# Optimization experiments

Hardware: AMD Instinct MI355X
Metric: run time of the kernel (lower is better)

Reference implementation:

```python
import jax, jax.numpy as jnp
import numpy as np

N_NODES = 200000
N_EDGES = 6400000
NUM_GRAPHS = 20000
D_NODE, D_EDGE, D_MSG = 5, 4, 10


def setup_inputs() -> dict:
    key = jax.random.key(0)
    ks = jax.random.split(key, 16)
    inp = {
        "edge_index": jax.random.randint(ks[0], (2, N_EDGES), 0, N_NODES, dtype=jnp.int64)
                      if jax.config.jax_enable_x64 else
                      jax.random.randint(ks[0], (2, N_EDGES), 0, N_NODES, dtype=jnp.int32),
        "node_attr": jax.random.normal(ks[1], (N_NODES, D_NODE), dtype=jnp.float32),
        "edge_attr": jax.random.normal(ks[2], (N_EDGES, D_EDGE), dtype=jnp.float32),
        "batch": jnp.sort(jax.random.randint(ks[3], (N_NODES,), 0, NUM_GRAPHS, dtype=jnp.int32)),
        "num_graphs": NUM_GRAPHS,
        # MPL_1: Linear(2*D_NODE + D_EDGE -> 10)
        "w_mpl": jax.random.normal(ks[4], (2 * D_NODE + D_EDGE, D_MSG), dtype=jnp.float32) * 0.3,
        "b_mpl": jnp.zeros((D_MSG,), dtype=jnp.float32),
        "w1": jax.random.normal(ks[5], (10, 10), dtype=jnp.float32) * 0.3,
        "b1": jnp.zeros((10,), dtype=jnp.float32),
        "w2": jax.random.normal(ks[6], (10, 5), dtype=jnp.float32) * 0.3,
        "b2": jnp.zeros((5,), dtype=jnp.float32),
        "w3": jax.random.normal(ks[7], (5, 5), dtype=jnp.float32) * 0.3,
        "b3": jnp.zeros((5,), dtype=jnp.float32),
        "w4": jax.random.normal(ks[8], (5, 1), dtype=jnp.float32) * 0.3,
        "b4": jnp.zeros((1,), dtype=jnp.float32),
    }
    return inp


def reference(edge_index, node_attr, edge_attr, batch, num_graphs,
              w_mpl, b_mpl, w1, b1, w2, b2, w3, b3, w4, b4):
    src, dst = edge_index[0], edge_index[1]
    n_nodes = node_attr.shape[0]
    # MPL_1: gather endpoints, concat with edge features, MLP, scatter-sum to dst
    edge_in = jnp.concatenate(
        [node_attr[src], node_attr[dst], edge_attr], axis=-1)  # [E, 14]
    msg = jax.nn.relu(edge_in @ w_mpl + b_mpl)                 # [E, 10]
    x = jax.ops.segment_sum(msg, dst, num_segments=n_nodes)    # [N, 10]
    # node MLP head
    x = jax.nn.relu(x @ w1 + b1)
    x = jax.nn.relu(x @ w2 + b2)
    # segment_coo(reduce='sum') over sorted batch index -> per-graph pooling
    x = jax.ops.segment_sum(x, batch, num_segments=num_graphs,
                            indices_are_sorted=True)           # [G, 5]
    x = jax.nn.relu(x @ w3 + b3)
    return x @ w4 + b4                                         # [G, 1]
```

## Files before the change

kernel.cpp:

```cpp
#include <hip/hip_runtime.h>

#define DN 5
#define DE 4
#define DM 10
#define NB 2048
#define BKT_SH 8
#define BKT_NODES 256
#define MAXBKT 1024

__global__ __launch_bounds__(256) void hist_pack_kernel(
    const int* __restrict__ ei, const float* __restrict__ node_attr,
    float4* __restrict__ napack, unsigned* __restrict__ cnt,
    int E, int chunk, int nbk, int N)
{
    __shared__ unsigned hist[MAXBKT];
    int t = threadIdx.x, b = blockIdx.x;

    int n = b * 256 + t;
    if (n < N) {
        const float* r = node_attr + (size_t)n * DN;
        napack[2 * (size_t)n]     = make_float4(r[0], r[1], r[2], r[3]);
        napack[2 * (size_t)n + 1] = make_float4(r[4], 0.f, 0.f, 0.f);
    }

    for (int j = t; j < nbk; j += 256) hist[j] = 0;
    __syncthreads();

    int e0 = b * chunk, e1 = min(E, e0 + chunk);
    for (int i = e0 + t; i < e1; i += 256) {
        int d = ei[(size_t)E + i];
        atomicAdd(&hist[d >> BKT_SH], 1u);
    }
    __syncthreads();
    for (int j = t; j < nbk; j += 256)
        cnt[(size_t)j * NB + b] = hist[j];
}

__global__ __launch_bounds__(256) void scan_rows_kernel(
    unsigned* __restrict__ cnt, unsigned* __restrict__ rowtotal)
{
    __shared__ unsigned lds[256];
    int j = blockIdx.x, t = threadIdx.x;
    unsigned* row = cnt + (size_t)j * NB;

    unsigned v[8], s = 0;
#pragma unroll
    for (int u = 0; u < 8; ++u) { v[u] = row[t * 8 + u]; s += v[u]; }
    lds[t] = s; __syncthreads();
#pragma unroll
    for (int o = 1; o < 256; o <<= 1) {
        unsigned add = (t >= o) ? lds[t - o] : 0u;
        __syncthreads();
        lds[t] += add;
        __syncthreads();
    }
    unsigned excl = lds[t] - s;
#pragma unroll
    for (int u = 0; u < 8; ++u) { row[t * 8 + u] = excl; excl += v[u]; }
    if (t == 255) rowtotal[j] = lds[255];
}

__global__ __launch_bounds__(1024) void scan_base_kernel(
    const unsigned* __restrict__ rowtotal, unsigned* __restrict__ gbase,
    int nbk, int E)
{
    __shared__ unsigned lds[1024];
    int t = threadIdx.x;
    unsigned v = (t < nbk) ? rowtotal[t] : 0u;
    lds[t] = v; __syncthreads();
#pragma unroll
    for (int o = 1; o < 1024; o <<= 1) {
        unsigned add = (t >= o) ? lds[t - o] : 0u;
        __syncthreads();
        lds[t] += add;
        __syncthreads();
    }
    unsigned excl = lds[t] - v;
    if (t < nbk)       gbase[t] = excl;
    else if (t == nbk) gbase[t] = (unsigned)E;
}

__global__ __launch_bounds__(256) void scatter_kernel(
    const int* __restrict__ ei, const float* __restrict__ edge_attr,
    const unsigned* __restrict__ cnt, const unsigned* __restrict__ gbase,
    float4* __restrict__ rec4, int E, int chunk, int nbk)
{
    __shared__ unsigned woff[MAXBKT];
    int t = threadIdx.x, b = blockIdx.x;
    for (int j = t; j < nbk; j += 256)
        woff[j] = gbase[j] + cnt[(size_t)j * NB + b];
    __syncthreads();

    int e0 = b * chunk, e1 = min(E, e0 + chunk);
    for (int i0 = e0 + t; i0 < e1; i0 += 4 * 256) {
        int s[4], d[4]; float4 ea[4]; bool act[4];
#pragma unroll
        for (int u = 0; u < 4; ++u) {
            int i = i0 + u * 256;
            act[u] = (i < e1);
            if (act[u]) {
                s[u] = ei[i];
                d[u] = ei[(size_t)E + i];
                ea[u] = reinterpret_cast<const float4*>(edge_attr)[i];
            }
        }
#pragma unroll
        for (int u = 0; u < 4; ++u) {
            if (!act[u]) continue;
            unsigned p = atomicAdd(&woff[d[u] >> BKT_SH], 1u);
            unsigned meta = (unsigned)s[u] | ((unsigned)(d[u] & 255) << 18);
            rec4[2 * (size_t)p]     = make_float4(__uint_as_float(meta), ea[u].x, ea[u].y, ea[u].z);
            rec4[2 * (size_t)p + 1] = make_float4(ea[u].w, 0.f, 0.f, 0.f);
        }
    }
}

__global__ __launch_bounds__(256) void gather_kernel(
    const float4* __restrict__ rec4, const unsigned* __restrict__ gbase,
    const float4* __restrict__ napack,
    const float* __restrict__ w_mpl, const float* __restrict__ b_mpl,
    float* __restrict__ xpart, size_t xstride,
    int E, int N, int nbk, int nsplit)
{
    __shared__ float acc[BKT_NODES * DM];
    __shared__ float pdl[BKT_NODES * 12];
    __shared__ float sws[50];
    __shared__ float swe[40];

    int t = threadIdx.x;
    int j  = blockIdx.x / nsplit;
    int sp = blockIdx.x - j * nsplit;
    int nb0 = j * BKT_NODES;

    if (t < 50)       sws[t] = w_mpl[t];
    else if (t < 90)  swe[t - 50] = w_mpl[100 + (t - 50)];

    for (int i = t; i < BKT_NODES * DM; i += 256) acc[i] = 0.f;

    {
        int n = nb0 + t;
        float a0 = 0.f, a1 = 0.f, a2 = 0.f, a3 = 0.f, a4 = 0.f;
        if (n < N) {
            float4 r0 = napack[2 * (size_t)n];
            float4 r1 = napack[2 * (size_t)n + 1];
            a0 = r0.x; a1 = r0.y; a2 = r0.z; a3 = r0.w; a4 = r1.x;
        }
#pragma unroll
        for (int q = 0; q < DM; ++q) {
            float v = b_mpl[q];
            v = fmaf(a0, w_mpl[50 + q], v);
            v = fmaf(a1, w_mpl[60 + q], v);
            v = fmaf(a2, w_mpl[70 + q], v);
            v = fmaf(a3, w_mpl[80 + q], v);
            v = fmaf(a4, w_mpl[90 + q], v);
            pdl[t * 12 + q] = v;
        }
    }
    __syncthreads();

    unsigned start = gbase[j];
    unsigned end   = gbase[j + 1];
    unsigned blen  = end - start;
    unsigned csz   = (blen + nsplit - 1) / nsplit;
    unsigned ss    = start + (unsigned)sp * csz;
    unsigned se    = min(end, ss + csz);

    for (unsigned i0 = ss + t; i0 < se; i0 += 4u * 256u) {
        float4 r0[4], r1[4]; bool act[4];
#pragma unroll
        for (int u = 0; u < 4; ++u) {
            unsigned i = i0 + (unsigned)u * 256u;
            act[u] = (i < se);
            if (act[u]) { r0[u] = rec4[2 * (size_t)i]; r1[u] = rec4[2 * (size_t)i + 1]; }
        }
        float4 n0[4], n1[4];
#pragma unroll
        for (int u = 0; u < 4; ++u)
            if (act[u]) {
                size_t s = __float_as_uint(r0[u].x) & 0x3FFFFu;
                n0[u] = napack[2 * s];
                n1[u] = napack[2 * s + 1];
            }
#pragma unroll
        for (int u = 0; u < 4; ++u) {
            if (!act[u]) continue;
            unsigned meta = __float_as_uint(r0[u].x);
            int dl = meta >> 18;
            const float* pr = &pdl[dl * 12];
            float4 p0 = *reinterpret_cast<const float4*>(pr);
            float4 p1 = *reinterpret_cast<const float4*>(pr + 4);
            float2 p2 = *reinterpret_cast<const float2*>(pr + 8);
            float m[DM] = {p0.x, p0.y, p0.z, p0.w, p1.x, p1.y, p1.z, p1.w, p2.x, p2.y};
            float a0 = n0[u].x, a1 = n0[u].y, a2 = n0[u].z, a3 = n0[u].w, a4 = n1[u].x;
            float e0 = r0[u].y, e1 = r0[u].z, e2 = r0[u].w, e3 = r1[u].x;
#pragma unroll
            for (int q = 0; q < DM; ++q) {
                float v = m[q];
                v = fmaf(a0, sws[q],      v);
                v = fmaf(a1, sws[10 + q], v);
                v = fmaf(a2, sws[20 + q], v);
                v = fmaf(a3, sws[30 + q], v);
                v = fmaf(a4, sws[40 + q], v);
                v = fmaf(e0, swe[q],      v);
                v = fmaf(e1, swe[10 + q], v);
                v = fmaf(e2, swe[20 + q], v);
                v = fmaf(e3, swe[30 + q], v);
                if (v > 0.f) atomicAdd(&acc[dl * DM + q], v);
            }
        }
    }
    __syncthreads();

    float* dst = xpart + (size_t)sp * xstride + (size_t)nb0 * DM;
    for (int i = t; i < BKT_NODES * DM; i += 256) dst[i] = acc[i];
}

__global__ __launch_bounds__(256) void combine_kernel(
    const float* __restrict__ xpart, size_t xstride,
    const int* __restrict__ batch,
    const float* __restrict__ w1, const float* __restrict__ b1,
    const float* __restrict__ w2, const float* __restrict__ b2,
    float* __restrict__ gacc, int N, int nsplit)
{
    __shared__ float s1[100], sb1[10], s2[50], sb2[5];
    int t = threadIdx.x;
    if (t < 100)      s1[t] = w1[t];
    else if (t < 110) sb1[t - 100] = b1[t - 100];
    else if (t < 160) s2[t - 110] = w2[t - 110];
    else if (t < 165) sb2[t - 160] = b2[t - 160];
    __syncthreads();

    int n = blockIdx.x * blockDim.x + t;
    bool valid = (n < N);
    int g = 0x7fffffff;
    float h2[5] = {0.f, 0.f, 0.f, 0.f, 0.f};

    if (valid) {
        float x[DM];
#pragma unroll
        for (int q = 0; q < DM; ++q) x[q] = 0.f;
        for (int sp = 0; sp < nsplit; ++sp) {
            const float2* row = reinterpret_cast<const float2*>(
                xpart + (size_t)sp * xstride + (size_t)n * DM);
#pragma unroll
            for (int h = 0; h < 5; ++h) {
                float2 v = row[h];
                x[2 * h] += v.x; x[2 * h + 1] += v.y;
            }
        }

        float h1[10];
#pragma unroll
        for (int q = 0; q < 10; ++q) h1[q] = sb1[q];
#pragma unroll
        for (int k = 0; k < 10; ++k)
#pragma unroll
            for (int q = 0; q < 10; ++q) h1[q] = fmaf(x[k], s1[k * 10 + q], h1[q]);
#pragma unroll
        for (int q = 0; q < 10; ++q) h1[q] = fmaxf(h1[q], 0.f);
#pragma unroll
        for (int q = 0; q < 5; ++q) h2[q] = sb2[q];
#pragma unroll
        for (int k = 0; k < 10; ++k)
#pragma unroll
            for (int q = 0; q < 5; ++q) h2[q] = fmaf(h1[k], s2[k * 5 + q], h2[q]);
#pragma unroll
        for (int q = 0; q < 5; ++q) h2[q] = fmaxf(h2[q], 0.f);
        g = batch[n];
    }

    int lane = t & 63;
#pragma unroll
    for (int o = 1; o < 64; o <<= 1) {
        int go = __shfl_down(g, o);
        float v0 = __shfl_down(h2[0], o);
        float v1 = __shfl_down(h2[1], o);
        float v2 = __shfl_down(h2[2], o);
        float v3 = __shfl_down(h2[3], o);
        float v4 = __shfl_down(h2[4], o);
        if (lane + o < 64 && go == g) {
            h2[0] += v0; h2[1] += v1; h2[2] += v2; h2[3] += v3; h2[4] += v4;
        }
    }
    int gp = __shfl_up(g, 1);
    bool head = (lane == 0) || (gp != g);
    if (head && g != 0x7fffffff) {
#pragma unroll
        for (int q = 0; q < 5; ++q)
            if (h2[q] != 0.f) unsafeAtomicAdd(&gacc[(size_t)g * 5 + q], h2[q]);
    }
}

__global__ __launch_bounds__(256) void graph_head_kernel(
    const float* __restrict__ gacc,
    const float* __restrict__ w3, const float* __restrict__ b3,
    const float* __restrict__ w4, const float* __restrict__ b4,
    float* __restrict__ out, int G)
{
    __shared__ float s3[25], sb3[5], s4[5], sb4[1];
    int t = threadIdx.x;
    if (t < 25)       s3[t] = w3[t];
    else if (t < 30)  sb3[t - 25] = b3[t - 25];
    else if (t < 35)  s4[t - 30] = w4[t - 30];
    else if (t == 35) sb4[0] = b4[0];
    __syncthreads();

    int g = blockIdx.x * blockDim.x + t;
    if (g >= G) return;

    float x[5];
#pragma unroll
    for (int k = 0; k < 5; ++k) x[k] = gacc[(size_t)g * 5 + k];

    float o = sb4[0];
#pragma unroll
    for (int q = 0; q < 5; ++q) {
        float h = sb3[q];
#pragma unroll
        for (int k = 0; k < 5; ++k) h = fmaf(x[k], s3[k * 5 + q], h);
        h = fmaxf(h, 0.f);
        o = fmaf(h, s4[q], o);
    }
    out[g] = o;
}

extern "C" void kernel_launch(void* const* d_in, const int* in_sizes, int n_in,
                              void* d_out, int out_size, void* d_ws, size_t ws_size,
                              hipStream_t stream)
{
    const int*   ei        = (const int*)d_in[0];
    const float* node_attr = (const float*)d_in[1];
    const float* edge_attr = (const float*)d_in[2];
    const int*   batch     = (const int*)d_in[3];
    const float* w_mpl = (const float*)d_in[5];
    const float* b_mpl = (const float*)d_in[6];
    const float* w1    = (const float*)d_in[7];
    const float* b1    = (const float*)d_in[8];
    const float* w2    = (const float*)d_in[9];
    const float* b2    = (const float*)d_in[10];
    const float* w3    = (const float*)d_in[11];
    const float* b3    = (const float*)d_in[12];
    const float* w4    = (const float*)d_in[13];
    const float* b4    = (const float*)d_in[14];
    float* out = (float*)d_out;

    const int E = in_sizes[0] / 2;
    const int N = in_sizes[1] / DN;
    const int G = out_size;

    const int nbk   = (N + BKT_NODES - 1) / BKT_NODES;
    const int chunk = (E + NB - 1) / NB;

    char* p = (char*)d_ws;
    float4*   rec4     = (float4*)p;   p += (size_t)E * 32;
    float4*   napack   = (float4*)p;   p += (size_t)N * 32;
    unsigned* rowtotal = (unsigned*)p; p += ((size_t)nbk * 4 + 15) & ~15ull;
    unsigned* gbase    = (unsigned*)p; p += ((size_t)(nbk + 1) * 4 + 15) & ~15ull;
    float*    gacc     = (float*)p;    p += (size_t)G * 5 * 4;
    unsigned* cnt      = (unsigned*)p;
    float*    xpart    = (float*)p;
    size_t cnt_bytes = (size_t)nbk * NB * 4;

    size_t used = (size_t)((char*)cnt - (char*)d_ws);
    size_t xstride = (size_t)nbk * BKT_NODES * DM;
    int nsplit = 8;
    while (nsplit > 1 &&
           used + ((cnt_bytes > (size_t)nsplit * xstride * 4) ? cnt_bytes
                                                              : (size_t)nsplit * xstride * 4) > ws_size)
        nsplit >>= 1;

    hipMemsetAsync(gacc, 0, (size_t)G * 5 * 4, stream);

    hist_pack_kernel<<<NB, 256, 0, stream>>>(ei, node_attr, napack, cnt, E, chunk, nbk, N);
    scan_rows_kernel<<<nbk, 256, 0, stream>>>(cnt, rowtotal);
    scan_base_kernel<<<1, 1024, 0, stream>>>(rowtotal, gbase, nbk, E);
    scatter_kernel<<<NB, 256, 0, stream>>>(ei, edge_attr, cnt, gbase, rec4, E, chunk, nbk);
    gather_kernel<<<nbk * nsplit, 256, 0, stream>>>(rec4, gbase, napack, w_mpl, b_mpl,
                                                    xpart, xstride, E, N, nbk, nsplit);
    combine_kernel<<<nbk, 256, 0, stream>>>(xpart, xstride, batch, w1, b1, w2, b2, gacc, N, nsplit);
    graph_head_kernel<<<(G + 255) / 256, 256, 0, stream>>>(gacc, w3, b3, w4, b4, out, G);
}
```

Measured before the change: 585.1 us.

## Prefetch source node features into edge records as fp16 during scatter

The scatter pass now gathers each edge's source-node features and stores them in the bucketed edge record alongside the edge attributes. Both are converted to half precision, so the gather pass no longer does random node lookups. Node packs shrink to 16 bytes, and nontemporal loads and stores are used for streaming data. This trades fp16 rounding of the inputs for fewer random reads and less data per record.

```diff
diff --git a/kernel.cpp b/kernel.cpp
--- a/kernel.cpp
+++ b/kernel.cpp
@@ -1,4 +1,5 @@
 #include <hip/hip_runtime.h>
+#include <hip/hip_fp16.h>
 
 #define DN 5
 #define DE 4
@@ -8,9 +9,21 @@
 #define BKT_NODES 256
 #define MAXBKT 1024
 
+typedef float        f4  __attribute__((ext_vector_type(4)));
+typedef unsigned int u4v __attribute__((ext_vector_type(4)));
+
+static __device__ __forceinline__ float2 h2f(unsigned u) {
+    __half2 h = *reinterpret_cast<__half2*>(&u);
+    return make_float2(__low2float(h), __high2float(h));
+}
+static __device__ __forceinline__ unsigned f2h(float a, float b) {
+    __half2 h = __floats2half2_rn(a, b);
+    return *reinterpret_cast<unsigned*>(&h);
+}
+
 __global__ __launch_bounds__(256) void hist_pack_kernel(
     const int* __restrict__ ei, const float* __restrict__ node_attr,
-    float4* __restrict__ napack, unsigned* __restrict__ cnt,
+    u4v* __restrict__ naph, unsigned* __restrict__ cnt,
     int E, int chunk, int nbk, int N)
 {
     __shared__ unsigned hist[MAXBKT];
@@ -19,8 +32,12 @@
     int n = b * 256 + t;
     if (n < N) {
         const float* r = node_attr + (size_t)n * DN;
-        napack[2 * (size_t)n]     = make_float4(r[0], r[1], r[2], r[3]);
-        napack[2 * (size_t)n + 1] = make_float4(r[4], 0.f, 0.f, 0.f);
+        u4v v;
+        v.x = f2h(r[0], r[1]);
+        v.y = f2h(r[2], r[3]);
+        v.z = f2h(r[4], 0.f);
+        v.w = 0u;
+        naph[n] = v;
     }
 
     for (int j = t; j < nbk; j += 256) hist[j] = 0;
@@ -28,7 +45,7 @@
 
     int e0 = b * chunk, e1 = min(E, e0 + chunk);
     for (int i = e0 + t; i < e1; i += 256) {
-        int d = ei[(size_t)E + i];
+        int d = __builtin_nontemporal_load(ei + (size_t)E + i);
         atomicAdd(&hist[d >> BKT_SH], 1u);
     }
     __syncthreads();
@@ -83,7 +100,8 @@
 __global__ __launch_bounds__(256) void scatter_kernel(
     const int* __restrict__ ei, const float* __restrict__ edge_attr,
     const unsigned* __restrict__ cnt, const unsigned* __restrict__ gbase,
-    float4* __restrict__ rec4, int E, int chunk, int nbk)
+    const u4v* __restrict__ naph,
+    f4* __restrict__ rec, int E, int chunk, int nbk)
 {
     __shared__ unsigned woff[MAXBKT];
     int t = threadIdx.x, b = blockIdx.x;
@@ -93,31 +111,43 @@
 
     int e0 = b * chunk, e1 = min(E, e0 + chunk);
     for (int i0 = e0 + t; i0 < e1; i0 += 4 * 256) {
-        int s[4], d[4]; float4 ea[4]; bool act[4];
+        int s[4], d[4]; f4 ea[4]; bool act[4];
 #pragma unroll
         for (int u = 0; u < 4; ++u) {
             int i = i0 + u * 256;
             act[u] = (i < e1);
             if (act[u]) {
-                s[u] = ei[i];
-                d[u] = ei[(size_t)E + i];
-                ea[u] = reinterpret_cast<const float4*>(edge_attr)[i];
+                s[u]  = __builtin_nontemporal_load(ei + i);
+                d[u]  = __builtin_nontemporal_load(ei + (size_t)E + i);
+                ea[u] = __builtin_nontemporal_load(
+                            reinterpret_cast<const f4*>(edge_attr) + i);
             }
         }
+        u4v nap[4];
+#pragma unroll
+        for (int u = 0; u < 4; ++u)
+            if (act[u]) nap[u] = naph[s[u]];
 #pragma unroll
         for (int u = 0; u < 4; ++u) {
             if (!act[u]) continue;
             unsigned p = atomicAdd(&woff[d[u] >> BKT_SH], 1u);
-            unsigned meta = (unsigned)s[u] | ((unsigned)(d[u] & 255) << 18);
-            rec4[2 * (size_t)p]     = make_float4(__uint_as_float(meta), ea[u].x, ea[u].y, ea[u].z);
-            rec4[2 * (size_t)p + 1] = make_float4(ea[u].w, 0.f, 0.f, 0.f);
+            f4 r0, r1;
+            r0.x = __uint_as_float((unsigned)(d[u] & 255));
+            r0.y = __uint_as_float(nap[u].x);
+            r0.z = __uint_as_float(nap[u].y);
+            r0.w = __uint_as_float(nap[u].z);
+            r1.x = __uint_as_float(f2h(ea[u].x, ea[u].y));
+            r1.y = __uint_as_float(f2h(ea[u].z, ea[u].w));
+            r1.z = 0.f; r1.w = 0.f;
+            __builtin_nontemporal_store(r0, rec + 2 * (size_t)p);
+            __builtin_nontemporal_store(r1, rec + 2 * (size_t)p + 1);
         }
     }
 }
 
 __global__ __launch_bounds__(256) void gather_kernel(
-    const float4* __restrict__ rec4, const unsigned* __restrict__ gbase,
-    const float4* __restrict__ napack,
+    const f4* __restrict__ rec, const unsigned* __restrict__ gbase,
+    const u4v* __restrict__ naph,
     const float* __restrict__ w_mpl, const float* __restrict__ b_mpl,
     float* __restrict__ xpart, size_t xstride,
     int E, int N, int nbk, int nsplit)
@@ -141,9 +171,9 @@
         int n = nb0 + t;
         float a0 = 0.f, a1 = 0.f, a2 = 0.f, a3 = 0.f, a4 = 0.f;
         if (n < N) {
-            float4 r0 = napack[2 * (size_t)n];
-            float4 r1 = napack[2 * (size_t)n + 1];
-            a0 = r0.x; a1 = r0.y; a2 = r0.z; a3 = r0.w; a4 = r1.x;
+            u4v v = naph[n];
+            float2 p01 = h2f(v.x), p23 = h2f(v.y), p4 = h2f(v.z);
+            a0 = p01.x; a1 = p01.y; a2 = p23.x; a3 = p23.y; a4 = p4.x;
         }
 #pragma unroll
         for (int q = 0; q < DM; ++q) {
@@ -166,33 +196,33 @@
     unsigned se    = min(end, ss + csz);
 
     for (unsigned i0 = ss + t; i0 < se; i0 += 4u * 256u) {
-        float4 r0[4], r1[4]; bool act[4];
+        f4 r0[4], r1[4]; bool act[4];
 #pragma unroll
         for (int u = 0; u < 4; ++u) {
             unsigned i = i0 + (unsigned)u * 256u;
             act[u] = (i < se);
-            if (act[u]) { r0[u] = rec4[2 * (size_t)i]; r1[u] = rec4[2 * (size_t)i + 1]; }
-        }
-        float4 n0[4], n1[4];
-#pragma unroll
-        for (int u = 0; u < 4; ++u)
             if (act[u]) {
-                size_t s = __float_as_uint(r0[u].x) & 0x3FFFFu;
-                n0[u] = napack[2 * s];
-                n1[u] = napack[2 * s + 1];
+                r0[u] = __builtin_nontemporal_load(rec + 2 * (size_t)i);
+                r1[u] = __builtin_nontemporal_load(rec + 2 * (size_t)i + 1);
             }
+        }
 #pragma unroll
         for (int u = 0; u < 4; ++u) {
             if (!act[u]) continue;
-            unsigned meta = __float_as_uint(r0[u].x);
-            int dl = meta >> 18;
+            int dl = (int)__float_as_uint(r0[u].x);
+            float2 s01 = h2f(__float_as_uint(r0[u].y));
+            float2 s23 = h2f(__float_as_uint(r0[u].z));
+            float2 s4_ = h2f(__float_as_uint(r0[u].w));
+            float2 e01 = h2f(__float_as_uint(r1[u].x));
+            float2 e23 = h2f(__float_as_uint(r1[u].y));
+            float a0 = s01.x, a1 = s01.y, a2 = s23.x, a3 = s23.y, a4 = s4_.x;
+            float e0 = e01.x, e1 = e01.y, e2 = e23.x, e3 = e23.y;
+
             const float* pr = &pdl[dl * 12];
             float4 p0 = *reinterpret_cast<const float4*>(pr);
             float4 p1 = *reinterpret_cast<const float4*>(pr + 4);
             float2 p2 = *reinterpret_cast<const float2*>(pr + 8);
             float m[DM] = {p0.x, p0.y, p0.z, p0.w, p1.x, p1.y, p1.z, p1.w, p2.x, p2.y};
-            float a0 = n0[u].x, a1 = n0[u].y, a2 = n0[u].z, a3 = n0[u].w, a4 = n1[u].x;
-            float e0 = r0[u].y, e1 = r0[u].z, e2 = r0[u].w, e3 = r1[u].x;
 #pragma unroll
             for (int q = 0; q < DM; ++q) {
                 float v = m[q];
@@ -212,7 +242,8 @@
     __syncthreads();
 
     float* dst = xpart + (size_t)sp * xstride + (size_t)nb0 * DM;
-    for (int i = t; i < BKT_NODES * DM; i += 256) dst[i] = acc[i];
+    for (int i = t; i < BKT_NODES * DM; i += 256)
+        __builtin_nontemporal_store(acc[i], dst + i);
 }
 
 __global__ __launch_bounds__(256) void combine_kernel(
@@ -352,8 +383,8 @@
     const int chunk = (E + NB - 1) / NB;
 
     char* p = (char*)d_ws;
-    float4*   rec4     = (float4*)p;   p += (size_t)E * 32;
-    float4*   napack   = (float4*)p;   p += (size_t)N * 32;
+    f4*       rec      = (f4*)p;       p += (size_t)E * 32;
+    u4v*      naph     = (u4v*)p;      p += (size_t)N * 16;
     unsigned* rowtotal = (unsigned*)p; p += ((size_t)nbk * 4 + 15) & ~15ull;
     unsigned* gbase    = (unsigned*)p; p += ((size_t)(nbk + 1) * 4 + 15) & ~15ull;
     float*    gacc     = (float*)p;    p += (size_t)G * 5 * 4;
@@ -371,11 +402,11 @@
 
     hipMemsetAsync(gacc, 0, (size_t)G * 5 * 4, stream);
 
-    hist_pack_kernel<<<NB, 256, 0, stream>>>(ei, node_attr, napack, cnt, E, chunk, nbk, N);
+    hist_pack_kernel<<<NB, 256, 0, stream>>>(ei, node_attr, naph, cnt, E, chunk, nbk, N);
     scan_rows_kernel<<<nbk, 256, 0, stream>>>(cnt, rowtotal);
     scan_base_kernel<<<1, 1024, 0, stream>>>(rowtotal, gbase, nbk, E);
-    scatter_kernel<<<NB, 256, 0, stream>>>(ei, edge_attr, cnt, gbase, rec4, E, chunk, nbk);
-    gather_kernel<<<nbk * nsplit, 256, 0, stream>>>(rec4, gbase, napack, w_mpl, b_mpl,
+    scatter_kernel<<<NB, 256, 0, stream>>>(ei, edge_attr, cnt, gbase, naph, rec, E, chunk, nbk);
+    gather_kernel<<<nbk * nsplit, 256, 0, stream>>>(rec, gbase, naph, w_mpl, b_mpl,
                                                     xpart, xstride, E, N, nbk, nsplit);
     combine_kernel<<<nbk, 256, 0, stream>>>(xpart, xstride, batch, w1, b1, w2, b2, gacc, N, nsplit);
     graph_head_kernel<<<(G + 255) / 256, 256, 0, stream>>>(gacc, w3, b3, w4, b4, out, G);
```

New measurement: 936.5 us. 60.0% more time.
